# Performance work log

Measured on AMD Instinct MI355X. Metric: run time of the kernel, lower is better.

## Reference

```python
import jax, jax.numpy as jnp
import numpy as np

PK_ROWS, PK_COLS = 256, 256
BATCH = 32
LSTM = 16
NEIGH = 8  # 8-neighborhood; input_size = NEIGH + 1
DYN_OUT = 1


def _build_grid_edges(rows, cols):
    """Replicates KernelNetwork.__init__ adjacency construction.
    Returns (pos0, coming_from, going_to) int arrays over directed grid edges.
    Direction codes 0..7: TL, T, TR, L, R, BL, B, BR (direction_dict - 1)."""
    offsets = [(-1, -1), (-1, 0), (-1, 1), (0, -1), (0, 1), (1, -1), (1, 0), (1, 1)]
    pos0, coming_from, going_to = [], [], []
    for r in range(rows):
        for c in range(cols):
            pid = r * cols + c
            for d, (dr, dc) in enumerate(offsets):
                nr, nc = r + dr, c + dc
                if 0 <= nr < rows and 0 <= nc < cols:
                    pos0.append(pid)
                    coming_from.append(nr * cols + nc)
                    going_to.append(d)
    return (np.asarray(pos0, np.int64), np.asarray(coming_from, np.int64),
            np.asarray(going_to, np.int64))


def setup_inputs() -> dict:
    key = jax.random.key(0)
    ks = jax.random.split(key, 10)
    P = PK_ROWS * PK_COLS
    pos0, coming_from, going_to = _build_grid_edges(PK_ROWS, PK_COLS)
    s = 0.1  # weight scale
    return {
        "dyn_in": jax.random.normal(ks[0], (BATCH, P), jnp.float32),
        "pk_lat_in": jax.random.normal(ks[1], (BATCH, P, NEIGH), jnp.float32),
        "pk_lat_out": jax.random.normal(ks[2], (BATCH, P, NEIGH), jnp.float32),
        "h": jax.random.normal(ks[3], (BATCH, P, LSTM), jnp.float32),
        "c": jax.random.normal(ks[4], (BATCH, P, LSTM), jnp.float32),
        "Wx": jax.random.normal(ks[5], (NEIGH + 1, 4 * LSTM), jnp.float32) * s,
        "Wh": jax.random.normal(ks[6], (LSTM, 4 * LSTM), jnp.float32) * s,
        "b": jnp.zeros((4 * LSTM,), jnp.float32),
        "Wo": jax.random.normal(ks[7], (LSTM, DYN_OUT + NEIGH), jnp.float32) * s,
        "bo": jnp.zeros((DYN_OUT + NEIGH,), jnp.float32),
        "pos0": jnp.asarray(pos0),
        "coming_from": jnp.asarray(coming_from),
        "going_to": jnp.asarray(going_to),
    }


def reference(dyn_in, pk_lat_in, pk_lat_out, h, c, Wx, Wh, b, Wo, bo,
              pos0, coming_from, going_to):
    # 1) lateral scatter-gather: route each PK's lateral output channel to the
    #    matching neighbor's lateral input slot (irregular gather + scatter).
    lat_in = pk_lat_in.at[:, pos0, going_to].set(
        pk_lat_out[:, coming_from, going_to])  # [B, P, 8]
    # 2) concat dynamic input channel with lateral inputs -> [B, P, 9]
    x = jnp.concatenate([dyn_in[:, :, None], lat_in], axis=2)
    # 3) parallel LSTM cell shared across all PKs
    gates = x @ Wx + h @ Wh + b  # [B, P, 4L]
    i, f, g, o = jnp.split(gates, 4, axis=-1)
    i, f, o = jax.nn.sigmoid(i), jax.nn.sigmoid(f), jax.nn.sigmoid(o)
    g = jnp.tanh(g)
    c_new = f * c + i * g
    h_new = o * jnp.tanh(c_new)
    # 4) output head -> [B, P, dyn_out + 8]; split into dynamic / lateral parts
    out = jnp.tanh(h_new @ Wo + bo)
    pk_dyn_out = out[:, :, :DYN_OUT]
    pk_lat_out_new = out[:, :, DYN_OUT:]
    return pk_dyn_out, pk_lat_out_new, h_new, c_new
```

## Files before the change

### kernel.cpp

```cpp
#include <hip/hip_runtime.h>

#define ROWS 256
#define COLS 256
#define NP (ROWS*COLS)
#define BATCH 32

#define WX_OFF 0
#define WH_OFF 576
#define B_OFF  1600
#define WO_OFF 1664
#define BO_OFF 1808
#define FLAG_OFF 1824

#define OUT_DYN 0
#define OUT_LAT 2097152
#define OUT_H   18874368
#define OUT_C   52428800

using u16 = unsigned short;
using u32 = unsigned int;

__device__ __forceinline__ float bf2f(u16 v){ return __uint_as_float(((u32)v) << 16); }
__device__ __forceinline__ u16 f2bf(float f){
    u32 u = __float_as_uint(f);
    return (u16)((u + 0x7fffu + ((u >> 16) & 1u)) >> 16);
}
__device__ __forceinline__ float rcpf_(float x){ return __builtin_amdgcn_rcpf(x); }
__device__ __forceinline__ float sigm(float x){ return rcpf_(1.f + __expf(-x)); }
__device__ __forceinline__ float tanh_(float x){ return 1.f - 2.f * rcpf_(1.f + __expf(2.f * x)); }
__device__ __forceinline__ void unpack2(u32 u, float& a, float& b){
    a = __uint_as_float(u << 16);
    b = __uint_as_float(u & 0xffff0000u);
}
__device__ __forceinline__ u32 pk2(float a, float b){
    return (u32)f2bf(a) | ((u32)f2bf(b) << 16);
}

__global__ void prep_weights(const void* __restrict__ Wx, const void* __restrict__ Wh,
                             const void* __restrict__ b,  const void* __restrict__ Wo,
                             const void* __restrict__ bo, float* __restrict__ ws){
    __shared__ int sflag;
    const int t = threadIdx.x;
    if (t == 0) sflag = 0;
    __syncthreads();
    float v = bf2f(((const u16*)Wx)[t]);
    if (!(fabsf(v) < 64.0f)) atomicOr(&sflag, 1);
    __syncthreads();
    const int f32in = sflag;

    for (int i = t; i < 576;  i += 256) ws[WX_OFF+i] = f32in ? ((const float*)Wx)[i] : bf2f(((const u16*)Wx)[i]);
    for (int i = t; i < 1024; i += 256) ws[WH_OFF+i] = f32in ? ((const float*)Wh)[i] : bf2f(((const u16*)Wh)[i]);
    for (int i = t; i < 64;   i += 256) ws[B_OFF+i]  = f32in ? ((const float*)b)[i]  : bf2f(((const u16*)b)[i]);
    for (int i = t; i < 144;  i += 256) ws[WO_OFF+i] = f32in ? ((const float*)Wo)[i] : bf2f(((const u16*)Wo)[i]);
    for (int i = t; i < 9;    i += 256) ws[BO_OFF+i] = f32in ? ((const float*)bo)[i] : bf2f(((const u16*)bo)[i]);
    if (t == 0) ((int*)ws)[FLAG_OFF] = f32in;
}

__global__ __launch_bounds__(256) void lstm_step(
    const void* __restrict__ dyn_in,
    const void* __restrict__ lat_in,
    const void* __restrict__ lat_out,
    const void* __restrict__ h_in,
    const void* __restrict__ c_in,
    const float* __restrict__ W,
    void* __restrict__ out)
{
    const int r   = blockIdx.x;
    const int bb  = blockIdx.y;
    const int col = threadIdx.x;
    const long base = (long)bb * NP + (long)r * COLS + col;
    const int f32in = ((const int*)W)[FLAG_OFF];

    __shared__ __align__(16) unsigned char latraw[3 * COLS * 8 * 4];

    const int drr[8] = {-1,-1,-1, 0, 0, 1, 1, 1};
    const int dcc[8] = {-1, 0, 1,-1, 1,-1, 0, 1};

    if (f32in){
        float* latf = (float*)latraw;
        #pragma unroll
        for (int rr = 0; rr < 3; rr++){
            int row = r + rr - 1;
            if (row >= 0 && row < ROWS){
                const uint4* s = (const uint4*)((const float*)lat_out + ((long)bb * NP + (long)row * COLS) * 8);
                uint4* d4 = (uint4*)(latf + (size_t)rr * COLS * 8);
                d4[col]       = s[col];
                d4[col + 256] = s[col + 256];
            }
        }
    } else {
        #pragma unroll
        for (int rr = 0; rr < 3; rr++){
            int row = r + rr - 1;
            if (row >= 0 && row < ROWS){
                const uint4* s = (const uint4*)((const u16*)lat_out + ((long)bb * NP + (long)row * COLS) * 8);
                ((uint4*)latraw)[rr * COLS + col] = s[col];
            }
        }
    }
    __syncthreads();

    float x[9], hv[16], cv[16];
    if (f32in){
        const float* latf = (const float*)latraw;
        x[0] = ((const float*)dyn_in)[base];
        #pragma unroll
        for (int d = 0; d < 8; d++){
            int nr = r + drr[d], nc = col + dcc[d];
            if (nr >= 0 && nr < ROWS && nc >= 0 && nc < COLS)
                x[1 + d] = latf[((drr[d] + 1) * COLS + nc) * 8 + d];
            else
                x[1 + d] = ((const float*)lat_in)[base * 8 + d];
        }
        const float4* hp = (const float4*)h_in + base * 4;
        const float4* cp = (const float4*)c_in + base * 4;
        #pragma unroll
        for (int q = 0; q < 4; q++){
            float4 hq = hp[q], cq = cp[q];
            hv[4*q+0]=hq.x; hv[4*q+1]=hq.y; hv[4*q+2]=hq.z; hv[4*q+3]=hq.w;
            cv[4*q+0]=cq.x; cv[4*q+1]=cq.y; cv[4*q+2]=cq.z; cv[4*q+3]=cq.w;
        }
    } else {
        const u16* lat = (const u16*)latraw;
        x[0] = bf2f(((const u16*)dyn_in)[base]);
        #pragma unroll
        for (int d = 0; d < 8; d++){
            int nr = r + drr[d], nc = col + dcc[d];
            if (nr >= 0 && nr < ROWS && nc >= 0 && nc < COLS)
                x[1 + d] = bf2f(lat[((drr[d] + 1) * COLS + nc) * 8 + d]);
            else
                x[1 + d] = bf2f(((const u16*)lat_in)[base * 8 + d]);
        }
        const uint4* hp = (const uint4*)h_in + base * 2;
        const uint4* cp = (const uint4*)c_in + base * 2;
        uint4 h0 = hp[0], h1 = hp[1], c0 = cp[0], c1 = cp[1];
        unpack2(h0.x, hv[0], hv[1]);  unpack2(h0.y, hv[2], hv[3]);
        unpack2(h0.z, hv[4], hv[5]);  unpack2(h0.w, hv[6], hv[7]);
        unpack2(h1.x, hv[8], hv[9]);  unpack2(h1.y, hv[10], hv[11]);
        unpack2(h1.z, hv[12], hv[13]);unpack2(h1.w, hv[14], hv[15]);
        unpack2(c0.x, cv[0], cv[1]);  unpack2(c0.y, cv[2], cv[3]);
        unpack2(c0.z, cv[4], cv[5]);  unpack2(c0.w, cv[6], cv[7]);
        unpack2(c1.x, cv[8], cv[9]);  unpack2(c1.y, cv[10], cv[11]);
        unpack2(c1.z, cv[12], cv[13]);unpack2(c1.w, cv[14], cv[15]);
    }

    float acc[64];
    #pragma unroll
    for (int j = 0; j < 64; j++) acc[j] = W[B_OFF + j];
    #pragma unroll
    for (int m = 0; m < 9; m++){
        float xm = x[m];
        #pragma unroll
        for (int j = 0; j < 64; j++) acc[j] = fmaf(xm, W[WX_OFF + m * 64 + j], acc[j]);
    }
    #pragma unroll
    for (int m = 0; m < 16; m++){
        float hm = hv[m];
        #pragma unroll
        for (int j = 0; j < 64; j++) acc[j] = fmaf(hm, W[WH_OFF + m * 64 + j], acc[j]);
    }

    float oacc[9];
    #pragma unroll
    for (int t = 0; t < 9; t++) oacc[t] = W[BO_OFF + t];
    float hn[16], cn[16];
    #pragma unroll
    for (int k = 0; k < 16; k++){
        float ig = sigm(acc[k]);
        float fg = sigm(acc[16 + k]);
        float gg = tanh_(acc[32 + k]);
        float og = sigm(acc[48 + k]);
        float c2 = fmaf(fg, cv[k], ig * gg);
        float h2 = og * tanh_(c2);
        cn[k] = c2; hn[k] = h2;
        #pragma unroll
        for (int t = 0; t < 9; t++) oacc[t] = fmaf(h2, W[WO_OFF + k * 9 + t], oacc[t]);
    }
    float dynout = tanh_(oacc[0]);
    float ov[8];
    #pragma unroll
    for (int t = 0; t < 8; t++) ov[t] = tanh_(oacc[1 + t]);

    if (f32in){
        float* of = (float*)out;
        of[OUT_DYN + base] = dynout;
        float4* lp = (float4*)(of + OUT_LAT) + base * 2;
        lp[0] = make_float4(ov[0], ov[1], ov[2], ov[3]);
        lp[1] = make_float4(ov[4], ov[5], ov[6], ov[7]);
        float4* hp2 = (float4*)(of + OUT_H) + base * 4;
        float4* cp2 = (float4*)(of + OUT_C) + base * 4;
        #pragma unroll
        for (int q = 0; q < 4; q++){
            hp2[q] = make_float4(hn[4*q], hn[4*q+1], hn[4*q+2], hn[4*q+3]);
            cp2[q] = make_float4(cn[4*q], cn[4*q+1], cn[4*q+2], cn[4*q+3]);
        }
    } else {
        u16* ob = (u16*)out;
        ob[OUT_DYN + base] = f2bf(dynout);
        *((uint4*)(ob + OUT_LAT) + base) =
            make_uint4(pk2(ov[0], ov[1]), pk2(ov[2], ov[3]), pk2(ov[4], ov[5]), pk2(ov[6], ov[7]));
        uint4* hop = (uint4*)(ob + OUT_H) + base * 2;
        hop[0] = make_uint4(pk2(hn[0], hn[1]), pk2(hn[2], hn[3]), pk2(hn[4], hn[5]), pk2(hn[6], hn[7]));
        hop[1] = make_uint4(pk2(hn[8], hn[9]), pk2(hn[10], hn[11]), pk2(hn[12], hn[13]), pk2(hn[14], hn[15]));
        uint4* cop = (uint4*)(ob + OUT_C) + base * 2;
        cop[0] = make_uint4(pk2(cn[0], cn[1]), pk2(cn[2], cn[3]), pk2(cn[4], cn[5]), pk2(cn[6], cn[7]));
        cop[1] = make_uint4(pk2(cn[8], cn[9]), pk2(cn[10], cn[11]), pk2(cn[12], cn[13]), pk2(cn[14], cn[15]));
    }
}

extern "C" void kernel_launch(void* const* d_in, const int* in_sizes, int n_in,
                              void* d_out, int out_size, void* d_ws, size_t ws_size,
                              hipStream_t stream){
    const void* dyn  = d_in[0];
    const void* lin  = d_in[1];
    const void* lout = d_in[2];
    const void* h    = d_in[3];
    const void* c    = d_in[4];
    const void* Wx   = d_in[5];
    const void* Wh   = d_in[6];
    const void* b    = d_in[7];
    const void* Wo   = d_in[8];
    const void* bo   = d_in[9];
    float* ws = (float*)d_ws;

    hipLaunchKernelGGL(prep_weights, dim3(1), dim3(256), 0, stream, Wx, Wh, b, Wo, bo, ws);
    hipLaunchKernelGGL(lstm_step, dim3(ROWS, BATCH), dim3(256), 0, stream,
                       dyn, lin, lout, h, c, ws, d_out);
}
```

Measured before the change: 645.5 us.

## Chunk LSTM gates per hidden quad, transpose lateral LDS, swizzle workgroups

The gate computation is split into four passes over groups of four hidden units. This drops the 64-float accumulator and the full c/h_new arrays, cutting register pressure so occupancy can rise. Each pass loads its own slice of c and streams out its own h/c results. The lateral shared-memory buffer becomes a direction-major float transpose so neighbour reads are stride-1 and conflict-free. Workgroup IDs are swizzled across batch/rows, and h loads are issued before the barrier. In exchange, the weights are reloaded per pass and the non-unrolled loop adds overhead.

New measurement: 764.9 us. +18.5%, slower.

```diff
diff --git a/kernel.cpp b/kernel.cpp
--- a/kernel.cpp
+++ b/kernel.cpp
@@ -65,27 +65,30 @@
     const float* __restrict__ W,
     void* __restrict__ out)
 {
-    const int r   = blockIdx.x;
-    const int bb  = blockIdx.y;
+    const int wg = blockIdx.y * gridDim.x + blockIdx.x;
+    const int sw = (wg & 7) * ((ROWS * BATCH) / 8) + (wg >> 3);
+    const int r   = sw & (ROWS - 1);
+    const int bb  = sw >> 8;
     const int col = threadIdx.x;
     const long base = (long)bb * NP + (long)r * COLS + col;
     const int f32in = ((const int*)W)[FLAG_OFF];
 
-    __shared__ __align__(16) unsigned char latraw[3 * COLS * 8 * 4];
+    __shared__ float lds[8][3][COLS];
 
     const int drr[8] = {-1,-1,-1, 0, 0, 1, 1, 1};
     const int dcc[8] = {-1, 0, 1,-1, 1,-1, 0, 1};
 
     if (f32in){
-        float* latf = (float*)latraw;
         #pragma unroll
         for (int rr = 0; rr < 3; rr++){
             int row = r + rr - 1;
             if (row >= 0 && row < ROWS){
-                const uint4* s = (const uint4*)((const float*)lat_out + ((long)bb * NP + (long)row * COLS) * 8);
-                uint4* d4 = (uint4*)(latf + (size_t)rr * COLS * 8);
-                d4[col]       = s[col];
-                d4[col + 256] = s[col + 256];
+                const float4* s = (const float4*)((const float*)lat_out + ((long)bb * NP + (long)row * COLS) * 8);
+                float4 a = s[2*col], b4 = s[2*col+1];
+                lds[0][rr][col] = a.x;  lds[1][rr][col] = a.y;
+                lds[2][rr][col] = a.z;  lds[3][rr][col] = a.w;
+                lds[4][rr][col] = b4.x; lds[5][rr][col] = b4.y;
+                lds[6][rr][col] = b4.z; lds[7][rr][col] = b4.w;
             }
         }
     } else {
@@ -94,88 +97,127 @@
             int row = r + rr - 1;
             if (row >= 0 && row < ROWS){
                 const uint4* s = (const uint4*)((const u16*)lat_out + ((long)bb * NP + (long)row * COLS) * 8);
-                ((uint4*)latraw)[rr * COLS + col] = s[col];
-            }
-        }
-    }
+                uint4 a = s[col];
+                float e0,e1,e2,e3,e4,e5,e6,e7;
+                unpack2(a.x, e0, e1); unpack2(a.y, e2, e3);
+                unpack2(a.z, e4, e5); unpack2(a.w, e6, e7);
+                lds[0][rr][col] = e0; lds[1][rr][col] = e1;
+                lds[2][rr][col] = e2; lds[3][rr][col] = e3;
+                lds[4][rr][col] = e4; lds[5][rr][col] = e5;
+                lds[6][rr][col] = e6; lds[7][rr][col] = e7;
+            }
+        }
+    }
+
+    float x[9], hv[16];
+    if (f32in){
+        x[0] = ((const float*)dyn_in)[base];
+        const float4* hp = (const float4*)h_in + base * 4;
+        #pragma unroll
+        for (int qq = 0; qq < 4; qq++){
+            float4 hq = hp[qq];
+            hv[4*qq+0]=hq.x; hv[4*qq+1]=hq.y; hv[4*qq+2]=hq.z; hv[4*qq+3]=hq.w;
+        }
+    } else {
+        x[0] = bf2f(((const u16*)dyn_in)[base]);
+        const uint4* hp = (const uint4*)h_in + base * 2;
+        uint4 h0 = hp[0], h1 = hp[1];
+        unpack2(h0.x, hv[0], hv[1]);   unpack2(h0.y, hv[2], hv[3]);
+        unpack2(h0.z, hv[4], hv[5]);   unpack2(h0.w, hv[6], hv[7]);
+        unpack2(h1.x, hv[8], hv[9]);   unpack2(h1.y, hv[10], hv[11]);
+        unpack2(h1.z, hv[12], hv[13]); unpack2(h1.w, hv[14], hv[15]);
+    }
+
     __syncthreads();
 
-    float x[9], hv[16], cv[16];
-    if (f32in){
-        const float* latf = (const float*)latraw;
-        x[0] = ((const float*)dyn_in)[base];
-        #pragma unroll
-        for (int d = 0; d < 8; d++){
-            int nr = r + drr[d], nc = col + dcc[d];
-            if (nr >= 0 && nr < ROWS && nc >= 0 && nc < COLS)
-                x[1 + d] = latf[((drr[d] + 1) * COLS + nc) * 8 + d];
-            else
-                x[1 + d] = ((const float*)lat_in)[base * 8 + d];
-        }
-        const float4* hp = (const float4*)h_in + base * 4;
-        const float4* cp = (const float4*)c_in + base * 4;
-        #pragma unroll
-        for (int q = 0; q < 4; q++){
-            float4 hq = hp[q], cq = cp[q];
-            hv[4*q+0]=hq.x; hv[4*q+1]=hq.y; hv[4*q+2]=hq.z; hv[4*q+3]=hq.w;
-            cv[4*q+0]=cq.x; cv[4*q+1]=cq.y; cv[4*q+2]=cq.z; cv[4*q+3]=cq.w;
-        }
-    } else {
-        const u16* lat = (const u16*)latraw;
-        x[0] = bf2f(((const u16*)dyn_in)[base]);
-        #pragma unroll
-        for (int d = 0; d < 8; d++){
-            int nr = r + drr[d], nc = col + dcc[d];
-            if (nr >= 0 && nr < ROWS && nc >= 0 && nc < COLS)
-                x[1 + d] = bf2f(lat[((drr[d] + 1) * COLS + nc) * 8 + d]);
-            else
-                x[1 + d] = bf2f(((const u16*)lat_in)[base * 8 + d]);
-        }
-        const uint4* hp = (const uint4*)h_in + base * 2;
-        const uint4* cp = (const uint4*)c_in + base * 2;
-        uint4 h0 = hp[0], h1 = hp[1], c0 = cp[0], c1 = cp[1];
-        unpack2(h0.x, hv[0], hv[1]);  unpack2(h0.y, hv[2], hv[3]);
-        unpack2(h0.z, hv[4], hv[5]);  unpack2(h0.w, hv[6], hv[7]);
-        unpack2(h1.x, hv[8], hv[9]);  unpack2(h1.y, hv[10], hv[11]);
-        unpack2(h1.z, hv[12], hv[13]);unpack2(h1.w, hv[14], hv[15]);
-        unpack2(c0.x, cv[0], cv[1]);  unpack2(c0.y, cv[2], cv[3]);
-        unpack2(c0.z, cv[4], cv[5]);  unpack2(c0.w, cv[6], cv[7]);
-        unpack2(c1.x, cv[8], cv[9]);  unpack2(c1.y, cv[10], cv[11]);
-        unpack2(c1.z, cv[12], cv[13]);unpack2(c1.w, cv[14], cv[15]);
-    }
-
-    float acc[64];
     #pragma unroll
-    for (int j = 0; j < 64; j++) acc[j] = W[B_OFF + j];
-    #pragma unroll
-    for (int m = 0; m < 9; m++){
-        float xm = x[m];
-        #pragma unroll
-        for (int j = 0; j < 64; j++) acc[j] = fmaf(xm, W[WX_OFF + m * 64 + j], acc[j]);
-    }
-    #pragma unroll
-    for (int m = 0; m < 16; m++){
-        float hm = hv[m];
-        #pragma unroll
-        for (int j = 0; j < 64; j++) acc[j] = fmaf(hm, W[WH_OFF + m * 64 + j], acc[j]);
+    for (int d = 0; d < 8; d++){
+        int nr = r + drr[d], nc = col + dcc[d];
+        if (nr >= 0 && nr < ROWS && nc >= 0 && nc < COLS){
+            x[1 + d] = lds[d][drr[d] + 1][nc];
+        } else {
+            x[1 + d] = f32in ? ((const float*)lat_in)[base * 8 + d]
+                             : bf2f(((const u16*)lat_in)[base * 8 + d]);
+        }
     }
 
     float oacc[9];
     #pragma unroll
     for (int t = 0; t < 9; t++) oacc[t] = W[BO_OFF + t];
-    float hn[16], cn[16];
-    #pragma unroll
-    for (int k = 0; k < 16; k++){
-        float ig = sigm(acc[k]);
-        float fg = sigm(acc[16 + k]);
-        float gg = tanh_(acc[32 + k]);
-        float og = sigm(acc[48 + k]);
-        float c2 = fmaf(fg, cv[k], ig * gg);
-        float h2 = og * tanh_(c2);
-        cn[k] = c2; hn[k] = h2;
-        #pragma unroll
-        for (int t = 0; t < 9; t++) oacc[t] = fmaf(h2, W[WO_OFF + k * 9 + t], oacc[t]);
-    }
+
+    #pragma unroll 1
+    for (int q = 0; q < 4; q++){
+        const int cb = 4 * q;
+
+        float cva, cvb, cvc, cvd;
+        if (f32in){
+            float4 cq = ((const float4*)c_in)[base * 4 + q];
+            cva = cq.x; cvb = cq.y; cvc = cq.z; cvd = cq.w;
+        } else {
+            uint2 cu = ((const uint2*)c_in)[base * 4 + q];
+            unpack2(cu.x, cva, cvb); unpack2(cu.y, cvc, cvd);
+        }
+
+        float ai[4], af[4], ag[4], ao[4];
+        #pragma unroll
+        for (int kk = 0; kk < 4; kk++){
+            ai[kk] = W[B_OFF + cb + kk];
+            af[kk] = W[B_OFF + 16 + cb + kk];
+            ag[kk] = W[B_OFF + 32 + cb + kk];
+            ao[kk] = W[B_OFF + 48 + cb + kk];
+        }
+        #pragma unroll
+        for (int m = 0; m < 9; m++){
+            const float xm = x[m];
+            const float* wb = W + WX_OFF + m * 64 + cb;
+            #pragma unroll
+            for (int kk = 0; kk < 4; kk++){
+                ai[kk] = fmaf(xm, wb[kk],      ai[kk]);
+                af[kk] = fmaf(xm, wb[16 + kk], af[kk]);
+                ag[kk] = fmaf(xm, wb[32 + kk], ag[kk]);
+                ao[kk] = fmaf(xm, wb[48 + kk], ao[kk]);
+            }
+        }
+        #pragma unroll
+        for (int m = 0; m < 16; m++){
+            const float hm = hv[m];
+            const float* wb = W + WH_OFF + m * 64 + cb;
+            #pragma unroll
+            for (int kk = 0; kk < 4; kk++){
+                ai[kk] = fmaf(hm, wb[kk],      ai[kk]);
+                af[kk] = fmaf(hm, wb[16 + kk], af[kk]);
+                ag[kk] = fmaf(hm, wb[32 + kk], ag[kk]);
+                ao[kk] = fmaf(hm, wb[48 + kk], ao[kk]);
+            }
+        }
+
+        const float cvv[4] = {cva, cvb, cvc, cvd};
+        float hn4[4], cn4[4];
+        #pragma unroll
+        for (int kk = 0; kk < 4; kk++){
+            float ig = sigm(ai[kk]);
+            float fg = sigm(af[kk]);
+            float gg = tanh_(ag[kk]);
+            float og = sigm(ao[kk]);
+            float cc = fmaf(fg, cvv[kk], ig * gg);
+            float hh = og * tanh_(cc);
+            cn4[kk] = cc; hn4[kk] = hh;
+            const float* wo = W + WO_OFF + (cb + kk) * 9;
+            #pragma unroll
+            for (int t = 0; t < 9; t++) oacc[t] = fmaf(hh, wo[t], oacc[t]);
+        }
+
+        if (f32in){
+            float* of = (float*)out;
+            ((float4*)(of + OUT_H))[base * 4 + q] = make_float4(hn4[0], hn4[1], hn4[2], hn4[3]);
+            ((float4*)(of + OUT_C))[base * 4 + q] = make_float4(cn4[0], cn4[1], cn4[2], cn4[3]);
+        } else {
+            u16* ob = (u16*)out;
+            ((uint2*)(ob + OUT_H))[base * 4 + q] = make_uint2(pk2(hn4[0], hn4[1]), pk2(hn4[2], hn4[3]));
+            ((uint2*)(ob + OUT_C))[base * 4 + q] = make_uint2(pk2(cn4[0], cn4[1]), pk2(cn4[2], cn4[3]));
+        }
+    }
+
     float dynout = tanh_(oacc[0]);
     float ov[8];
     #pragma unroll
@@ -187,24 +229,11 @@
         float4* lp = (float4*)(of + OUT_LAT) + base * 2;
         lp[0] = make_float4(ov[0], ov[1], ov[2], ov[3]);
         lp[1] = make_float4(ov[4], ov[5], ov[6], ov[7]);
-        float4* hp2 = (float4*)(of + OUT_H) + base * 4;
-        float4* cp2 = (float4*)(of + OUT_C) + base * 4;
-        #pragma unroll
-        for (int q = 0; q < 4; q++){
-            hp2[q] = make_float4(hn[4*q], hn[4*q+1], hn[4*q+2], hn[4*q+3]);
-            cp2[q] = make_float4(cn[4*q], cn[4*q+1], cn[4*q+2], cn[4*q+3]);
-        }
     } else {
         u16* ob = (u16*)out;
         ob[OUT_DYN + base] = f2bf(dynout);
         *((uint4*)(ob + OUT_LAT) + base) =
             make_uint4(pk2(ov[0], ov[1]), pk2(ov[2], ov[3]), pk2(ov[4], ov[5]), pk2(ov[6], ov[7]));
-        uint4* hop = (uint4*)(ob + OUT_H) + base * 2;
-        hop[0] = make_uint4(pk2(hn[0], hn[1]), pk2(hn[2], hn[3]), pk2(hn[4], hn[5]), pk2(hn[6], hn[7]));
-        hop[1] = make_uint4(pk2(hn[8], hn[9]), pk2(hn[10], hn[11]), pk2(hn[12], hn[13]), pk2(hn[14], hn[15]));
-        uint4* cop = (uint4*)(ob + OUT_C) + base * 2;
-        cop[0] = make_uint4(pk2(cn[0], cn[1]), pk2(cn[2], cn[3]), pk2(cn[4], cn[5]), pk2(cn[6], cn[7]));
-        cop[1] = make_uint4(pk2(cn[8], cn[9]), pk2(cn[10], cn[11]), pk2(cn[12], cn[13]), pk2(cn[14], cn[15]));
     }
 }
 
```
